# Optimization experiments

Hardware: AMD Instinct MI355X
Metric: run time of the kernel (lower is better)

Reference implementation:

```python
import jax, jax.numpy as jnp
import numpy as np

B, N, D, STK_TOTAL = 8, 2048, 128, 4000


def setup_inputs() -> dict:
    key = jax.random.key(0)
    k1, k2, k3, k4 = jax.random.split(key, 4)
    x = jax.random.normal(k1, (B, N, D), dtype=jnp.float32)
    stk_ten = jax.random.randint(k2, (B, N), 0, STK_TOTAL, dtype=jnp.int32)
    # learned parameter tables (trained state; original inits: ones / xavier-uniform)
    stk_matrix = jax.random.normal(k3, (STK_TOTAL, STK_TOTAL), dtype=jnp.float32)
    stk_weight = jax.random.normal(k4, (STK_TOTAL, STK_TOTAL), dtype=jnp.float32)
    return {"x": x, "stk_ten": stk_ten, "stk_matrix": stk_matrix, "stk_weight": stk_weight}


def reference(x, stk_ten, stk_matrix, stk_weight):
    # x: [B, N, D]; stk_ten: [B, N] int ids < STK_TOTAL
    idx = stk_ten.astype(jnp.int32)
    # per-batch double gather -> [B, N, N] submatrices (vectorized index_select x2)
    M = stk_matrix[idx[:, :, None], idx[:, None, :]]          # [B, N, N]
    W = jnp.abs(stk_weight[idx[:, :, None], idx[:, None, :]])  # [B, N, N]
    n = idx.shape[1]
    eye = jnp.eye(n, dtype=bool)                               # diag removal mask
    M = jnp.where(eye, jnp.float32(0.0), M)                    # stk_m_s - diag_embed(diag)
    W = jnp.where(eye, jnp.float32(0.0), W)
    # dropout is identity in inference mode (training=False)
    att = jax.nn.softmax(W, axis=2)                            # [B, N, N]
    out = jnp.matmul(M * att, x)                               # [B, N, D]
    return out
```

## Files before the change

### kernel.cpp

```cpp
#include <hip/hip_runtime.h>
#include <math.h>

#define BATCH 8
#define N 2048
#define D 128
#define ST 4000

#define BI 32
#define TJ 64
#define NT 256
#define NITER (N / TJ)
#define TJP 72

typedef short bf16x8 __attribute__((ext_vector_type(8)));
typedef float f32x16 __attribute__((ext_vector_type(16)));

__device__ __forceinline__ unsigned short f2bf(float f) {
    union { float f; unsigned u; } v; v.f = f;
    const unsigned r = v.u + 0x7FFFu + ((v.u >> 16) & 1u);
    return (unsigned short)(r >> 16);
}

__global__ __launch_bounds__(1024) void sort_kernel(
    const int* __restrict__ stk_ten,
    int* __restrict__ sval,
    int* __restrict__ spos)
{
    __shared__ unsigned keys[N];
    const int b = blockIdx.x;
    const int t = threadIdx.x;
    const int* idxb = stk_ten + b * N;
    for (int j = t; j < N; j += 1024)
        keys[j] = ((unsigned)idxb[j] << 11) | (unsigned)j;
    __syncthreads();
    for (int k = 2; k <= N; k <<= 1) {
        for (int jj = k >> 1; jj > 0; jj >>= 1) {
            for (int ix = t; ix < N; ix += 1024) {
                const int ixj = ix ^ jj;
                if (ixj > ix) {
                    const unsigned a = keys[ix], c = keys[ixj];
                    const bool up = ((ix & k) == 0);
                    if ((a > c) == up) { keys[ix] = c; keys[ixj] = a; }
                }
            }
            __syncthreads();
        }
    }
    for (int j = t; j < N; j += 1024) {
        const unsigned kk = keys[j];
        sval[b * N + j] = (int)(kk >> 11);
        spos[b * N + j] = (int)(kk & 2047u);
    }
}

__global__ __launch_bounds__(256) void xt_kernel(
    const float* __restrict__ x,
    const int* __restrict__ spos,
    unsigned short* __restrict__ xT)
{
    __shared__ float xs[TJ][129];
    __shared__ int sp_s[TJ];
    const int t  = threadIdx.x;
    const int b  = blockIdx.x >> 5;
    const int jt = blockIdx.x & 31;
    const int j0 = jt * TJ;
    if (t < TJ) sp_s[t] = spos[b * N + j0 + t];
    __syncthreads();
    const int tx = t & 31, ty = t >> 5;
    const float* xb = x + (size_t)b * N * D;
    #pragma unroll
    for (int p = 0; p < 8; ++p) {
        const int r = ty + 8 * p;
        const float* src = xb + (size_t)sp_s[r] * D;
        #pragma unroll
        for (int i = 0; i < 4; ++i)
            xs[r][tx + 32 * i] = src[tx + 32 * i];
    }
    __syncthreads();
    const int jp = t & 31, dd0 = t >> 5;
    unsigned short* xTb = xT + (size_t)b * D * N;
    #pragma unroll
    for (int q = 0; q < 16; ++q) {
        const int dd = dd0 + 8 * q;
        const unsigned lo = f2bf(xs[2 * jp][dd]);
        const unsigned hi = f2bf(xs[2 * jp + 1][dd]);
        *(unsigned*)(xTb + (size_t)dd * N + j0 + 2 * jp) = (hi << 16) | lo;
    }
}

__global__ __launch_bounds__(NT, 2) void fused_kernel(
    const unsigned short* __restrict__ xT,
    const int* __restrict__ stk_ten,
    const float* __restrict__ stk_matrix,
    const float* __restrict__ stk_weight,
    const int* __restrict__ sval,
    const int* __restrict__ spos,
    float* __restrict__ out)
{
    __shared__ __align__(16) unsigned short xs[D * TJP];
    __shared__ __align__(16) unsigned short cs[BI * TJP];
    __shared__ int   sv_s[2][TJ], sp_s[2][TJ], ri_s[BI];
    __shared__ float l_s[BI];

    const int t    = threadIdx.x;
    const int b    = blockIdx.x >> 6;
    const int i0   = (blockIdx.x & 63) * BI;
    const int lane = t & 63;
    const int w    = t >> 6;

    if (t < BI) ri_s[t] = stk_ten[b * N + i0 + t];
    const int* svb = sval + b * N;
    const int* spb = spos + b * N;
    if (t < TJ) { sv_s[0][t] = svb[t]; sp_s[0][t] = spb[t]; }
    __syncthreads();

    int cj = sv_s[0][lane], pj = sp_s[0][lane];
    float mg[8], wv[8];
    #pragma unroll
    for (int k = 0; k < 8; ++k) {
        const size_t off = (size_t)ri_s[w + 4 * k] * ST + cj;
        mg[k] = stk_matrix[off];
        wv[k] = stk_weight[off];
    }

    f32x16 acc;
    #pragma unroll
    for (int r = 0; r < 16; ++r) acc[r] = 0.0f;
    float l_run[8] = {0, 0, 0, 0, 0, 0, 0, 0};

    const unsigned short* xTb = xT + (size_t)b * D * N;

    for (int jt = 0; jt < NITER; ++jt) {
        const int nb = (jt & 1) ^ 1;
        const int j0 = jt * TJ;

        #pragma unroll
        for (int p = 0; p < 4; ++p) {
            const int c = t + p * 256;
            const int row = c >> 3, cno = c & 7;
            *(uint4*)(xs + row * TJP + cno * 8) =
                *(const uint4*)(xTb + (size_t)row * N + j0 + cno * 8);
        }
        if (jt + 1 < NITER && t < TJ) {
            sv_s[nb][t] = svb[j0 + TJ + t];
            sp_s[nb][t] = spb[j0 + TJ + t];
        }
        #pragma unroll
        for (int k = 0; k < 8; ++k) {
            const int row = w + 4 * k;
            const bool diag = (pj == i0 + row);
            const float ww = diag ? 0.0f : fabsf(wv[k]);
            const float e = __expf(ww);
            const float c = diag ? 0.0f : mg[k] * e;
            cs[row * TJP + lane] = f2bf(c);
            float s = e;
            #pragma unroll
            for (int dd = 1; dd < 64; dd <<= 1) s += __shfl_xor(s, dd, 64);
            l_run[k] += s;
        }
        __syncthreads();

        if (jt + 1 < NITER) {
            cj = sv_s[nb][lane]; pj = sp_s[nb][lane];
            #pragma unroll
            for (int k = 0; k < 8; ++k) {
                const size_t off = (size_t)ri_s[w + 4 * k] * ST + cj;
                mg[k] = stk_matrix[off];
                wv[k] = stk_weight[off];
            }
        }

        #pragma unroll
        for (int ks = 0; ks < 4; ++ks) {
            const bf16x8 av = *(const bf16x8*)(cs + (lane & 31) * TJP + ks * 16 + (lane >> 5) * 8);
            const bf16x8 bv = *(const bf16x8*)(xs + (32 * w + (lane & 31)) * TJP + ks * 16 + (lane >> 5) * 8);
            acc = __builtin_amdgcn_mfma_f32_32x32x16_bf16(av, bv, acc, 0, 0, 0);
        }
        __syncthreads();
    }

    #pragma unroll
    for (int k = 0; k < 8; ++k)
        if (lane == k) l_s[w + 4 * k] = l_run[k];
    __syncthreads();

    const int col = lane & 31, q2 = lane >> 5;
    #pragma unroll
    for (int r = 0; r < 16; ++r) {
        const int row = (r & 3) + 8 * (r >> 2) + 4 * q2;
        const float linv = 1.0f / l_s[row];
        out[((size_t)(b * N + i0 + row) << 7) + 32 * w + col] = acc[r] * linv;
    }
}

extern "C" void kernel_launch(void* const* d_in, const int* in_sizes, int n_in,
                              void* d_out, int out_size, void* d_ws, size_t ws_size,
                              hipStream_t stream) {
    const float* x          = (const float*)d_in[0];
    const int*   stk_ten    = (const int*)d_in[1];
    const float* stk_matrix = (const float*)d_in[2];
    const float* stk_weight = (const float*)d_in[3];
    float* out = (float*)d_out;

    int* sval = (int*)d_ws;
    int* spos = sval + BATCH * N;
    unsigned short* xT = (unsigned short*)(spos + BATCH * N);

    sort_kernel<<<BATCH, 1024, 0, stream>>>(stk_ten, sval, spos);
    xt_kernel<<<BATCH * (N / TJ), 256, 0, stream>>>(x, spos, xT);
    fused_kernel<<<BATCH * (N / BI), NT, 0, stream>>>(
        xT, stk_ten, stk_matrix, stk_weight, sval, spos, out);
}
```

Measured before the change: 259.2 us.

## Pack matrix and weight tables into bf16/fp16 pairs, counting-sort ids, split-K fused kernel

Adds a pack kernel that converts stk_matrix to bf16 and |stk_weight| to fp16 and interleaves them into one 32-bit word per entry, so each gather in the fused kernel is a single 4-byte load instead of two. The bitonic sort is replaced by a counting sort over the 4000 ids. The fused kernel is reorganized: 16 query rows per block, each wave handles a quarter of the columns with 16x16x32 MFMAs, loads x directly from global memory with no LDS staging or block barriers, and the partial sums are reduced through shared memory at the end. The pack pass streams the full 4000x4000 tables on every call, which is extra traffic, and storing the weight in fp16 lowers the precision of the softmax input.

```diff
diff --git a/kernel.cpp b/kernel.cpp
--- a/kernel.cpp
+++ b/kernel.cpp
@@ -1,4 +1,5 @@
 #include <hip/hip_runtime.h>
+#include <hip/hip_fp16.h>
 #include <math.h>
 
 #define BATCH 8
@@ -6,14 +7,13 @@
 #define D 128
 #define ST 4000
 
-#define BI 32
 #define TJ 64
-#define NT 256
-#define NITER (N / TJ)
-#define TJP 72
+#define IT 16
+#define KQ 4
+#define TPW 8
 
 typedef short bf16x8 __attribute__((ext_vector_type(8)));
-typedef float f32x16 __attribute__((ext_vector_type(16)));
+typedef float f32x4  __attribute__((ext_vector_type(4)));
 
 __device__ __forceinline__ unsigned short f2bf(float f) {
     union { float f; unsigned u; } v; v.f = f;
@@ -21,35 +21,82 @@
     return (unsigned short)(r >> 16);
 }
 
+__global__ __launch_bounds__(256) void pack_kernel(
+    const float* __restrict__ M, const float* __restrict__ W,
+    unsigned* __restrict__ P)
+{
+    const size_t i4 = ((size_t)blockIdx.x * 256 + threadIdx.x) * 4;
+    const float4 m4 = *(const float4*)(M + i4);
+    const float4 w4 = *(const float4*)(W + i4);
+    uint4 o;
+    o.x = ((unsigned)f2bf(m4.x) << 16) | (unsigned)__half_as_ushort(__float2half(fabsf(w4.x)));
+    o.y = ((unsigned)f2bf(m4.y) << 16) | (unsigned)__half_as_ushort(__float2half(fabsf(w4.y)));
+    o.z = ((unsigned)f2bf(m4.z) << 16) | (unsigned)__half_as_ushort(__float2half(fabsf(w4.z)));
+    o.w = ((unsigned)f2bf(m4.w) << 16) | (unsigned)__half_as_ushort(__float2half(fabsf(w4.w)));
+    *(uint4*)(P + i4) = o;
+}
+
 __global__ __launch_bounds__(1024) void sort_kernel(
     const int* __restrict__ stk_ten,
     int* __restrict__ sval,
     int* __restrict__ spos)
 {
-    __shared__ unsigned keys[N];
-    const int b = blockIdx.x;
-    const int t = threadIdx.x;
+    __shared__ int hist[4000];
+    __shared__ int base[4000];
+    __shared__ int wsum[16];
+    const int b = blockIdx.x, t = threadIdx.x;
+    const int lane = t & 63, wv = t >> 6;
     const int* idxb = stk_ten + b * N;
-    for (int j = t; j < N; j += 1024)
-        keys[j] = ((unsigned)idxb[j] << 11) | (unsigned)j;
-    __syncthreads();
-    for (int k = 2; k <= N; k <<= 1) {
-        for (int jj = k >> 1; jj > 0; jj >>= 1) {
-            for (int ix = t; ix < N; ix += 1024) {
-                const int ixj = ix ^ jj;
-                if (ixj > ix) {
-                    const unsigned a = keys[ix], c = keys[ixj];
-                    const bool up = ((ix & k) == 0);
-                    if ((a > c) == up) { keys[ix] = c; keys[ixj] = a; }
-                }
-            }
-            __syncthreads();
+
+    for (int j = t; j < 4000; j += 1024) hist[j] = 0;
+    __syncthreads();
+    const int v0 = idxb[t], v1 = idxb[t + 1024];
+    atomicAdd(&hist[v0], 1);
+    atomicAdd(&hist[v1], 1);
+    __syncthreads();
+
+    int h[4], c[4], run = 0;
+    #pragma unroll
+    for (int i = 0; i < 4; ++i) {
+        const int bi = 4 * t + i;
+        h[i] = (bi < 4000) ? hist[bi] : 0;
+        run += h[i];
+        c[i] = run;
+    }
+    const int tsum = run;
+    int incl = tsum;
+    #pragma unroll
+    for (int d = 1; d < 64; d <<= 1) {
+        const int tmp = __shfl_up(incl, d, 64);
+        if (lane >= d) incl += tmp;
+    }
+    if (lane == 63) wsum[wv] = incl;
+    __syncthreads();
+    if (t < 16) {
+        const int v = wsum[t];
+        int iv = v;
+        #pragma unroll
+        for (int d = 1; d < 16; d <<= 1) {
+            const int tmp = __shfl_up(iv, d, 64);
+            if (lane >= d) iv += tmp;
         }
-    }
-    for (int j = t; j < N; j += 1024) {
-        const unsigned kk = keys[j];
-        sval[b * N + j] = (int)(kk >> 11);
-        spos[b * N + j] = (int)(kk & 2047u);
+        wsum[t] = iv - v;
+    }
+    __syncthreads();
+    const int ex = incl - tsum + wsum[wv];
+    #pragma unroll
+    for (int i = 0; i < 4; ++i) {
+        const int bi = 4 * t + i;
+        if (bi < 4000) base[bi] = ex + c[i] - h[i];
+    }
+    __syncthreads();
+    for (int j = t; j < 4000; j += 1024) hist[j] = 0;
+    __syncthreads();
+    {
+        const int p0 = base[v0] + atomicAdd(&hist[v0], 1);
+        sval[b * N + p0] = v0; spos[b * N + p0] = t;
+        const int p1 = base[v1] + atomicAdd(&hist[v1], 1);
+        sval[b * N + p1] = v1; spos[b * N + p1] = t + 1024;
     }
 }
 
@@ -88,108 +135,129 @@
     }
 }
 
-__global__ __launch_bounds__(NT, 2) void fused_kernel(
+__global__ __launch_bounds__(256, 2) void fused_kernel(
     const unsigned short* __restrict__ xT,
     const int* __restrict__ stk_ten,
-    const float* __restrict__ stk_matrix,
-    const float* __restrict__ stk_weight,
+    const unsigned* __restrict__ P,
     const int* __restrict__ sval,
     const int* __restrict__ spos,
     float* __restrict__ out)
 {
-    __shared__ __align__(16) unsigned short xs[D * TJP];
-    __shared__ __align__(16) unsigned short cs[BI * TJP];
-    __shared__ int   sv_s[2][TJ], sp_s[2][TJ], ri_s[BI];
-    __shared__ float l_s[BI];
+    __shared__ __align__(16) unsigned short cs[KQ][IT * 72];
+    __shared__ float accbuf[KQ][IT][136];
+    __shared__ float lbuf[KQ][IT];
+    __shared__ int ri_s[IT];
 
     const int t    = threadIdx.x;
-    const int b    = blockIdx.x >> 6;
-    const int i0   = (blockIdx.x & 63) * BI;
     const int lane = t & 63;
     const int w    = t >> 6;
-
-    if (t < BI) ri_s[t] = stk_ten[b * N + i0 + t];
+    const int b    = blockIdx.x >> 7;
+    const int i0   = (blockIdx.x & 127) * IT;
+
+    if (t < IT) ri_s[t] = stk_ten[b * N + i0 + t];
+    __syncthreads();
+
+    unsigned rowoff[IT];
+    #pragma unroll
+    for (int m = 0; m < IT; ++m) rowoff[m] = (unsigned)ri_s[m] * ST;
+
     const int* svb = sval + b * N;
     const int* spb = spos + b * N;
-    if (t < TJ) { sv_s[0][t] = svb[t]; sp_s[0][t] = spb[t]; }
-    __syncthreads();
-
-    int cj = sv_s[0][lane], pj = sp_s[0][lane];
-    float mg[8], wv[8];
-    #pragma unroll
-    for (int k = 0; k < 8; ++k) {
-        const size_t off = (size_t)ri_s[w + 4 * k] * ST + cj;
-        mg[k] = stk_matrix[off];
-        wv[k] = stk_weight[off];
-    }
-
-    f32x16 acc;
-    #pragma unroll
-    for (int r = 0; r < 16; ++r) acc[r] = 0.0f;
-    float l_run[8] = {0, 0, 0, 0, 0, 0, 0, 0};
-
     const unsigned short* xTb = xT + (size_t)b * D * N;
-
-    for (int jt = 0; jt < NITER; ++jt) {
-        const int nb = (jt & 1) ^ 1;
-        const int j0 = jt * TJ;
-
-        #pragma unroll
-        for (int p = 0; p < 4; ++p) {
-            const int c = t + p * 256;
-            const int row = c >> 3, cno = c & 7;
-            *(uint4*)(xs + row * TJP + cno * 8) =
-                *(const uint4*)(xTb + (size_t)row * N + j0 + cno * 8);
+    unsigned short* csw = &cs[w][0];
+
+    f32x4 acc[8];
+    #pragma unroll
+    for (int nb = 0; nb < 8; ++nb)
+        #pragma unroll
+        for (int r = 0; r < 4; ++r) acc[nb][r] = 0.0f;
+    float l_part[IT];
+    #pragma unroll
+    for (int m = 0; m < IT; ++m) l_part[m] = 0.0f;
+
+    const int jbase = w * (TPW * TJ);
+    const int brow  = lane & 15;
+    const int bcol  = (lane >> 4) * 8;
+
+    int cj = svb[jbase + lane];
+    int pj = spb[jbase + lane];
+    unsigned gv[IT];
+    #pragma unroll
+    for (int m = 0; m < IT; ++m) gv[m] = P[rowoff[m] + (unsigned)cj];
+
+    for (int tt = 0; tt < TPW; ++tt) {
+        const int j0  = jbase + tt * TJ;
+        const int j0n = (tt == TPW - 1) ? jbase : j0 + TJ;
+
+        const int cjn = svb[j0n + lane];
+        const int pjn = spb[j0n + lane];
+        uint4 bv[8];
+        #pragma unroll
+        for (int nb = 0; nb < 8; ++nb)
+            bv[nb] = *(const uint4*)(xTb + (size_t)(nb * 16 + brow) * N + j0 + bcol);
+
+        #pragma unroll
+        for (int m = 0; m < IT; ++m) {
+            const unsigned u = gv[m];
+            const float mf = __uint_as_float(u & 0xFFFF0000u);
+            const float wf = __half2float(__ushort_as_half((unsigned short)(u & 0xFFFFu)));
+            const bool diag = (pj == i0 + m);
+            const float e = diag ? 1.0f : __expf(wf);
+            l_part[m] += e;
+            const float c = diag ? 0.0f : mf * e;
+            csw[m * 72 + lane] = f2bf(c);
         }
-        if (jt + 1 < NITER && t < TJ) {
-            sv_s[nb][t] = svb[j0 + TJ + t];
-            sp_s[nb][t] = spb[j0 + TJ + t];
+
+        const bf16x8 av0 = *(const bf16x8*)(csw + brow * 72 + bcol);
+        const bf16x8 av1 = *(const bf16x8*)(csw + brow * 72 + 32 + bcol);
+
+        unsigned gvn[IT];
+        #pragma unroll
+        for (int m = 0; m < IT; ++m) gvn[m] = P[rowoff[m] + (unsigned)cjn];
+
+        #pragma unroll
+        for (int nb = 0; nb < 8; ++nb)
+            acc[nb] = __builtin_amdgcn_mfma_f32_16x16x32_bf16(
+                av0, *(const bf16x8*)&bv[nb], acc[nb], 0, 0, 0);
+        #pragma unroll
+        for (int nb = 0; nb < 8; ++nb)
+            bv[nb] = *(const uint4*)(xTb + (size_t)(nb * 16 + brow) * N + j0 + 32 + bcol);
+        #pragma unroll
+        for (int nb = 0; nb < 8; ++nb)
+            acc[nb] = __builtin_amdgcn_mfma_f32_16x16x32_bf16(
+                av1, *(const bf16x8*)&bv[nb], acc[nb], 0, 0, 0);
+
+        #pragma unroll
+        for (int m = 0; m < IT; ++m) gv[m] = gvn[m];
+        cj = cjn; pj = pjn;
+    }
+
+    #pragma unroll
+    for (int m = 0; m < IT; ++m) {
+        float v = l_part[m];
+        #pragma unroll
+        for (int d = 1; d < 64; d <<= 1) v += __shfl_xor(v, d, 64);
+        if (lane == 0) lbuf[w][m] = v;
+    }
+    #pragma unroll
+    for (int nb = 0; nb < 8; ++nb)
+        #pragma unroll
+        for (int r = 0; r < 4; ++r)
+            accbuf[w][(lane >> 4) * 4 + r][nb * 16 + (lane & 15)] = acc[nb][r];
+    __syncthreads();
+
+    #pragma unroll
+    for (int rr = 0; rr < 4; ++rr) {
+        const int row = 4 * w + rr;
+        const float linv = 1.0f /
+            (lbuf[0][row] + lbuf[1][row] + lbuf[2][row] + lbuf[3][row]);
+        #pragma unroll
+        for (int p = 0; p < 2; ++p) {
+            const int dd = lane + 64 * p;
+            const float s = accbuf[0][row][dd] + accbuf[1][row][dd] +
+                            accbuf[2][row][dd] + accbuf[3][row][dd];
+            out[((size_t)(b * N + i0 + row) << 7) + dd] = s * linv;
         }
-        #pragma unroll
-        for (int k = 0; k < 8; ++k) {
-            const int row = w + 4 * k;
-            const bool diag = (pj == i0 + row);
-            const float ww = diag ? 0.0f : fabsf(wv[k]);
-            const float e = __expf(ww);
-            const float c = diag ? 0.0f : mg[k] * e;
-            cs[row * TJP + lane] = f2bf(c);
-            float s = e;
-            #pragma unroll
-            for (int dd = 1; dd < 64; dd <<= 1) s += __shfl_xor(s, dd, 64);
-            l_run[k] += s;
-        }
-        __syncthreads();
-
-        if (jt + 1 < NITER) {
-            cj = sv_s[nb][lane]; pj = sp_s[nb][lane];
-            #pragma unroll
-            for (int k = 0; k < 8; ++k) {
-                const size_t off = (size_t)ri_s[w + 4 * k] * ST + cj;
-                mg[k] = stk_matrix[off];
-                wv[k] = stk_weight[off];
-            }
-        }
-
-        #pragma unroll
-        for (int ks = 0; ks < 4; ++ks) {
-            const bf16x8 av = *(const bf16x8*)(cs + (lane & 31) * TJP + ks * 16 + (lane >> 5) * 8);
-            const bf16x8 bv = *(const bf16x8*)(xs + (32 * w + (lane & 31)) * TJP + ks * 16 + (lane >> 5) * 8);
-            acc = __builtin_amdgcn_mfma_f32_32x32x16_bf16(av, bv, acc, 0, 0, 0);
-        }
-        __syncthreads();
-    }
-
-    #pragma unroll
-    for (int k = 0; k < 8; ++k)
-        if (lane == k) l_s[w + 4 * k] = l_run[k];
-    __syncthreads();
-
-    const int col = lane & 31, q2 = lane >> 5;
-    #pragma unroll
-    for (int r = 0; r < 16; ++r) {
-        const int row = (r & 3) + 8 * (r >> 2) + 4 * q2;
-        const float linv = 1.0f / l_s[row];
-        out[((size_t)(b * N + i0 + row) << 7) + 32 * w + col] = acc[r] * linv;
     }
 }
 
@@ -202,12 +270,14 @@
     const float* stk_weight = (const float*)d_in[3];
     float* out = (float*)d_out;
 
-    int* sval = (int*)d_ws;
+    unsigned* P = (unsigned*)d_ws;
+    int* sval = (int*)(P + (size_t)ST * ST);
     int* spos = sval + BATCH * N;
     unsigned short* xT = (unsigned short*)(spos + BATCH * N);
 
+    pack_kernel<<<(ST * ST) / 1024, 256, 0, stream>>>(stk_matrix, stk_weight, P);
     sort_kernel<<<BATCH, 1024, 0, stream>>>(stk_ten, sval, spos);
     xt_kernel<<<BATCH * (N / TJ), 256, 0, stream>>>(x, spos, xT);
-    fused_kernel<<<BATCH * (N / BI), NT, 0, stream>>>(
-        xT, stk_ten, stk_matrix, stk_weight, sval, spos, out);
-}
+    fused_kernel<<<BATCH * (N / IT), 256, 0, stream>>>(
+        xT, stk_ten, P, sval, spos, out);
+}
```

Measured after the change: 243.5 us. 6.1% less time.
